# Performance work log

Hardware: AMD Instinct MI355X
Metric: run time of the kernel (lower is better)

Reference implementation:

```python
import jax, jax.numpy as jnp
import numpy as np


def _splat(img_bhwc, y0, y1, x0, x1):
    """Integral-image corner scatter: each source pixel adds its value over the
    inclusive rect [y0,y1]x[x0,x1] by writing signed deltas at 4 corners.
    The later double-cumsum turns these deltas into the box sums.
    Returns (count, img_acc) of shapes (b,h,w) and (b,h,w,c)."""
    b, h, w, c = img_bhwc.shape
    dt = img_bhwc.dtype
    y0c = jnp.maximum(y0, 0)
    x0c = jnp.maximum(x0, 0)
    yp = y1 + 1  # exclusive bottom row
    xp = x1 + 1  # exclusive right col
    my = (yp < h)
    mx = (xp < w)
    one = jnp.ones(y0c.shape, dt)
    zero = jnp.zeros(y0c.shape, dt)
    ypc = jnp.minimum(yp, h - 1)
    xpc = jnp.minimum(xp, w - 1)
    corners = [
        (y0c, x0c, one),
        (y0c, xpc, jnp.where(mx, -one, zero)),
        (ypc, x0c, jnp.where(my, -one, zero)),
        (ypc, xpc, jnp.where(my & mx, one, zero)),
    ]
    bidx = jnp.arange(b)[:, None, None]
    pix = img_bhwc.reshape(b * h * w, c)  # per-source-pixel splat value
    cnt = jnp.zeros((b * h * w,), dt)
    acc = jnp.zeros((b * h * w, c), dt)
    for yy, xx, wgt in corners:  # fixed 4-corner loop, not a data-dim loop
        idx = ((bidx * h + yy) * w + xx).reshape(-1)
        wf = wgt.reshape(-1)
        cnt = cnt.at[idx].add(wf)
        acc = acc.at[idx].add(wf[:, None] * pix)
    return cnt.reshape(b, h, w), acc.reshape(b, h, w, c)


def _finalize(cnt, img_acc):
    # integral image over (h, w), clamp count to >=1, average, clip to [0,1]
    cf = jnp.cumsum(jnp.cumsum(cnt, axis=1), axis=2)
    cf = jnp.maximum(cf, 1.0)
    av = jnp.cumsum(jnp.cumsum(img_acc, axis=1), axis=2) / cf[..., None]
    return jnp.clip(av, 0.0, 1.0)


def reference(image, depth):
    b, c, h, w = image.shape
    img = jnp.transpose(image, (0, 2, 3, 1))  # b,h,w,c
    R = jnp.floor(depth).astype(jnp.int32)  # splat radius in pixels (b,h,w)
    ys = jnp.arange(h)[:, None]
    xs = jnp.arange(w)[None, :]
    y0 = ys - R
    y1 = ys + R
    xc = jnp.broadcast_to(xs, R.shape)
    # left view: rect shifted left of the pixel; right view: shifted right
    cnt_l, acc_l = _splat(img, y0, y1, xc - 2 * R, xc)
    cnt_r, acc_r = _splat(img, y0, y1, xc, xc + 2 * R)
    img_left_avg = jnp.transpose(_finalize(cnt_l, acc_l), (0, 3, 1, 2))
    img_right_avg = jnp.transpose(_finalize(cnt_r, acc_r), (0, 3, 1, 2))
    return img_left_avg, img_right_avg


def setup_inputs() -> dict:
    key = jax.random.key(0)
    k1, k2 = jax.random.split(key)
    B, C, H, W = 8, 3, 1024, 1024
    MAX_DISP = 8.0  # max circle-of-confusion radius in pixels
    image = jax.random.uniform(k1, (B, C, H, W), dtype=jnp.float32)
    depth = jax.random.uniform(k2, (B, H, W), dtype=jnp.float32) * MAX_DISP
    return {"image": image, "depth": depth}
```

## Files before the change

### kernel.cpp

```cpp
#include <hip/hip_runtime.h>


typedef _Float16 h_t;
typedef _Float16 h4 __attribute__((ext_vector_type(4)));

constexpr int Hh = 1024, Ww = 1024, Bb = 8, Cc = 3;
constexpr int NCOL = 256;
constexpr int HALO = 14;
constexpr int TWD  = NCOL - 2 * HALO;
constexpr int STRIP = 32;
constexpr int RING = 17;

__device__ __forceinline__ float sat01(float x) {
  return fminf(fmaxf(x, 0.0f), 1.0f);
}

__device__ __forceinline__ int mod_ring(int y) {
  int m = y % RING;
  return m < 0 ? m + RING : m;
}

__global__ __launch_bounds__(256)
void coc_vsep(const float* __restrict__ img, const float* __restrict__ dep,
              float* __restrict__ out) {
  __shared__ h4 ring[RING * NCOL];
  __shared__ h4 Sb[8 * NCOL];

  const int c  = threadIdx.x;
  const int X0 = blockIdx.x * TWD;
  const int Y0 = blockIdx.y * STRIP;
  const int b  = blockIdx.z;
  const int x  = X0 - HALO + c;
  const size_t plane = (size_t)Hh * Ww;
  const float* db = dep + (size_t)b * plane;
  const float* ib = img + (size_t)b * Cc * plane;

  auto stage = [&](int y) {
    h4 v = {(h_t)0.f, (h_t)0.f, (h_t)0.f, (h_t)-1.f};
    if ((unsigned)y < (unsigned)Hh && (unsigned)x < (unsigned)Ww) {
      size_t p = (size_t)y * Ww + x;
      v.x = (h_t)ib[p];
      v.y = (h_t)ib[plane + p];
      v.z = (h_t)ib[2 * plane + p];
      v.w = (h_t)floorf(db[p]);
    }
    ring[mod_ring(y) * NCOL + c] = v;
  };

  for (int y = Y0 - 8; y <= Y0 + 8; ++y) stage(y);
  __syncthreads();

  float4 C[8];
  #pragma unroll
  for (int t = 0; t < 8; ++t) C[t] = make_float4(0.f, 0.f, 0.f, 0.f);
  #pragma unroll
  for (int d = -7; d <= 7; ++d) {
    h4 tx = ring[mod_ring(Y0 - 1 + d) * NCOL + c];
    float R = (float)tx.w;
    const int ad = d < 0 ? -d : d;
    #pragma unroll
    for (int t = ad; t < 8; ++t) {
      float m = sat01(1.0f - fabsf(R - (float)t));
      C[t].x = fmaf(m, (float)tx.x, C[t].x);
      C[t].y = fmaf(m, (float)tx.y, C[t].y);
      C[t].z = fmaf(m, (float)tx.z, C[t].z);
      C[t].w += m;
    }
  }

  int sY = mod_ring(Y0);
  for (int r = 0; r < STRIP; ++r) {
    const int Y = Y0 + r;

    #pragma unroll
    for (int t = 0; t < 8; ++t) {
      int si = sY + t;      si -= (si >= RING) ? RING : 0;
      int so = sY - 1 - t;  so += (so < 0) ? RING : 0;
      h4 ti = ring[si * NCOL + c];
      h4 to = ring[so * NCOL + c];
      float mi = sat01(1.0f - fabsf((float)ti.w - (float)t));
      float mo = sat01(1.0f - fabsf((float)to.w - (float)t));
      C[t].x = fmaf(mi, (float)ti.x, C[t].x);
      C[t].y = fmaf(mi, (float)ti.y, C[t].y);
      C[t].z = fmaf(mi, (float)ti.z, C[t].z);
      C[t].w += mi;
      C[t].x = fmaf(-mo, (float)to.x, C[t].x);
      C[t].y = fmaf(-mo, (float)to.y, C[t].y);
      C[t].z = fmaf(-mo, (float)to.z, C[t].z);
      C[t].w -= mo;
    }
    {
      float ax = 0.f, ay = 0.f, az = 0.f, aw = 0.f;
      #pragma unroll
      for (int t = 7; t >= 0; --t) {
        ax += C[t].x; ay += C[t].y; az += C[t].z; aw += C[t].w;
        h4 sv = {(h_t)ax, (h_t)ay, (h_t)az, (h_t)aw};
        Sb[t * NCOL + c] = sv;
      }
    }
    __syncthreads();

    if (c < TWD && (X0 + c) < Ww) {
      const int a = c + HALO;
      h4 s0 = Sb[0 * NCOL + a];
      float lx = (float)s0.x, ly = (float)s0.y, lz = (float)s0.z, lw = (float)s0.w;
      float rx = lx, ry = ly, rz = lz, rw = lw;
      #pragma unroll
      for (int k = 1; k <= 7; ++k) {
        h4 l0 = Sb[k * NCOL + a + 2 * k - 1];
        h4 l1 = Sb[k * NCOL + a + 2 * k];
        h4 r0 = Sb[k * NCOL + a - 2 * k];
        h4 r1 = Sb[k * NCOL + a - 2 * k + 1];
        lx += (float)l0.x + (float)l1.x;
        ly += (float)l0.y + (float)l1.y;
        lz += (float)l0.z + (float)l1.z;
        lw += (float)l0.w + (float)l1.w;
        rx += (float)r0.x + (float)r1.x;
        ry += (float)r0.y + (float)r1.y;
        rz += (float)r0.z + (float)r1.z;
        rw += (float)r0.w + (float)r1.w;
      }
      const int X = X0 + c;
      size_t p = (size_t)Y * Ww + X;
      float* outL = out + (size_t)b * Cc * plane;
      float* outR = out + (size_t)(Bb + b) * Cc * plane;
      float invL = 1.0f / fmaxf(lw, 1.0f);
      float invR = 1.0f / fmaxf(rw, 1.0f);
      outL[p]             = sat01(lx * invL);
      outL[plane + p]     = sat01(ly * invL);
      outL[2 * plane + p] = sat01(lz * invL);
      outR[p]             = sat01(rx * invR);
      outR[plane + p]     = sat01(ry * invR);
      outR[2 * plane + p] = sat01(rz * invR);
    }
    stage(Y + 9);
    __syncthreads();

    sY += 1; sY -= (sY >= RING) ? RING : 0;
  }
}

extern "C" void kernel_launch(void* const* d_in, const int* in_sizes, int n_in,
                              void* d_out, int out_size, void* d_ws, size_t ws_size,
                              hipStream_t stream) {
  const float* img = (const float*)d_in[0];
  const float* dep = (const float*)d_in[1];
  float* out = (float*)d_out;
  dim3 grid((Ww + TWD - 1) / TWD, Hh / STRIP, Bb);
  dim3 block(NCOL, 1, 1);
  hipLaunchKernelGGL(coc_vsep, grid, block, 0, stream, img, dep, out);
}
```

Before: 427.8 us.

## Replace shared-memory row ring with per-thread register sliding window

The 17-row shared-memory ring of staged pixels is replaced by a 16-entry per-thread register window, since each thread only reads its own column. The next row's global load is issued at the top of each iteration so it can overlap the accumulation. Depth is now held in fp32 registers instead of fp16. In exchange the kernel uses many more VGPRs for the window and register shifts, which may lower occupancy, and it keeps two barriers per row around the Sb writes.

Result: faster. 418.1 us (-2.3%).

```diff
diff --git a/kernel.cpp b/kernel.cpp
--- a/kernel.cpp
+++ b/kernel.cpp
@@ -9,21 +9,14 @@
 constexpr int HALO = 14;
 constexpr int TWD  = NCOL - 2 * HALO;
 constexpr int STRIP = 32;
-constexpr int RING = 17;
 
 __device__ __forceinline__ float sat01(float x) {
   return fminf(fmaxf(x, 0.0f), 1.0f);
 }
 
-__device__ __forceinline__ int mod_ring(int y) {
-  int m = y % RING;
-  return m < 0 ? m + RING : m;
-}
-
 __global__ __launch_bounds__(256)
 void coc_vsep(const float* __restrict__ img, const float* __restrict__ dep,
               float* __restrict__ out) {
-  __shared__ h4 ring[RING * NCOL];
   __shared__ h4 Sb[8 * NCOL];
 
   const int c  = threadIdx.x;
@@ -34,109 +27,119 @@
   const size_t plane = (size_t)Hh * Ww;
   const float* db = dep + (size_t)b * plane;
   const float* ib = img + (size_t)b * Cc * plane;
+  const bool xok = (unsigned)x < (unsigned)Ww;
 
-  auto stage = [&](int y) {
-    h4 v = {(h_t)0.f, (h_t)0.f, (h_t)0.f, (h_t)-1.f};
-    if ((unsigned)y < (unsigned)Hh && (unsigned)x < (unsigned)Ww) {
+  h4    Tc[16];
+  float Tr[16];
+
+  auto loadrow = [&](int y, h4& rgb, float& R) {
+    rgb = (h4){(h_t)0.f, (h_t)0.f, (h_t)0.f, (h_t)0.f};
+    R = -1.0f;
+    if ((unsigned)y < (unsigned)Hh && xok) {
       size_t p = (size_t)y * Ww + x;
-      v.x = (h_t)ib[p];
-      v.y = (h_t)ib[plane + p];
-      v.z = (h_t)ib[2 * plane + p];
-      v.w = (h_t)floorf(db[p]);
+      rgb.x = (h_t)ib[p];
+      rgb.y = (h_t)ib[plane + p];
+      rgb.z = (h_t)ib[2 * plane + p];
+      R = floorf(db[p]);
     }
-    ring[mod_ring(y) * NCOL + c] = v;
   };
 
-  for (int y = Y0 - 8; y <= Y0 + 8; ++y) stage(y);
-  __syncthreads();
+  #pragma unroll
+  for (int d = 0; d < 16; ++d) loadrow(Y0 - 8 + d, Tc[d], Tr[d]);
 
   float4 C[8];
   #pragma unroll
   for (int t = 0; t < 8; ++t) C[t] = make_float4(0.f, 0.f, 0.f, 0.f);
   #pragma unroll
   for (int d = -7; d <= 7; ++d) {
-    h4 tx = ring[mod_ring(Y0 - 1 + d) * NCOL + c];
-    float R = (float)tx.w;
+    const int i = 7 + d;
     const int ad = d < 0 ? -d : d;
     #pragma unroll
     for (int t = ad; t < 8; ++t) {
-      float m = sat01(1.0f - fabsf(R - (float)t));
-      C[t].x = fmaf(m, (float)tx.x, C[t].x);
-      C[t].y = fmaf(m, (float)tx.y, C[t].y);
-      C[t].z = fmaf(m, (float)tx.z, C[t].z);
+      float m = sat01(1.0f - fabsf(Tr[i] - (float)t));
+      C[t].x = fmaf(m, (float)Tc[i].x, C[t].x);
+      C[t].y = fmaf(m, (float)Tc[i].y, C[t].y);
+      C[t].z = fmaf(m, (float)Tc[i].z, C[t].z);
       C[t].w += m;
     }
   }
 
-  int sY = mod_ring(Y0);
+  float* outL = out + (size_t)b * Cc * plane;
+  float* outR = out + (size_t)(Bb + b) * Cc * plane;
+
+  #pragma unroll 2
   for (int r = 0; r < STRIP; ++r) {
     const int Y = Y0 + r;
+    h4 nc; float nr;
+    loadrow(Y + 8, nc, nr);
 
     #pragma unroll
     for (int t = 0; t < 8; ++t) {
-      int si = sY + t;      si -= (si >= RING) ? RING : 0;
-      int so = sY - 1 - t;  so += (so < 0) ? RING : 0;
-      h4 ti = ring[si * NCOL + c];
-      h4 to = ring[so * NCOL + c];
-      float mi = sat01(1.0f - fabsf((float)ti.w - (float)t));
-      float mo = sat01(1.0f - fabsf((float)to.w - (float)t));
-      C[t].x = fmaf(mi, (float)ti.x, C[t].x);
-      C[t].y = fmaf(mi, (float)ti.y, C[t].y);
-      C[t].z = fmaf(mi, (float)ti.z, C[t].z);
+      const int ii = 8 + t, io = 7 - t;
+      float mi = sat01(1.0f - fabsf(Tr[ii] - (float)t));
+      float mo = sat01(1.0f - fabsf(Tr[io] - (float)t));
+      C[t].x = fmaf(mi, (float)Tc[ii].x, C[t].x);
+      C[t].y = fmaf(mi, (float)Tc[ii].y, C[t].y);
+      C[t].z = fmaf(mi, (float)Tc[ii].z, C[t].z);
       C[t].w += mi;
-      C[t].x = fmaf(-mo, (float)to.x, C[t].x);
-      C[t].y = fmaf(-mo, (float)to.y, C[t].y);
-      C[t].z = fmaf(-mo, (float)to.z, C[t].z);
+      C[t].x = fmaf(-mo, (float)Tc[io].x, C[t].x);
+      C[t].y = fmaf(-mo, (float)Tc[io].y, C[t].y);
+      C[t].z = fmaf(-mo, (float)Tc[io].z, C[t].z);
       C[t].w -= mo;
     }
+
+    h4 sv[8];
     {
       float ax = 0.f, ay = 0.f, az = 0.f, aw = 0.f;
       #pragma unroll
       for (int t = 7; t >= 0; --t) {
         ax += C[t].x; ay += C[t].y; az += C[t].z; aw += C[t].w;
-        h4 sv = {(h_t)ax, (h_t)ay, (h_t)az, (h_t)aw};
-        Sb[t * NCOL + c] = sv;
+        sv[t] = (h4){(h_t)ax, (h_t)ay, (h_t)az, (h_t)aw};
       }
     }
+
+    __syncthreads();
+    #pragma unroll
+    for (int t = 0; t < 8; ++t) Sb[t * NCOL + c] = sv[t];
     __syncthreads();
 
     if (c < TWD && (X0 + c) < Ww) {
       const int a = c + HALO;
-      h4 s0 = Sb[0 * NCOL + a];
-      float lx = (float)s0.x, ly = (float)s0.y, lz = (float)s0.z, lw = (float)s0.w;
-      float rx = lx, ry = ly, rz = lz, rw = lw;
+      float4 L, Rv;
+      {
+        h4 s0 = Sb[a];
+        L.x = (float)s0.x; L.y = (float)s0.y; L.z = (float)s0.z; L.w = (float)s0.w;
+        Rv = L;
+      }
       #pragma unroll
       for (int k = 1; k <= 7; ++k) {
         h4 l0 = Sb[k * NCOL + a + 2 * k - 1];
         h4 l1 = Sb[k * NCOL + a + 2 * k];
         h4 r0 = Sb[k * NCOL + a - 2 * k];
         h4 r1 = Sb[k * NCOL + a - 2 * k + 1];
-        lx += (float)l0.x + (float)l1.x;
-        ly += (float)l0.y + (float)l1.y;
-        lz += (float)l0.z + (float)l1.z;
-        lw += (float)l0.w + (float)l1.w;
-        rx += (float)r0.x + (float)r1.x;
-        ry += (float)r0.y + (float)r1.y;
-        rz += (float)r0.z + (float)r1.z;
-        rw += (float)r0.w + (float)r1.w;
+        L.x += (float)l0.x + (float)l1.x;
+        L.y += (float)l0.y + (float)l1.y;
+        L.z += (float)l0.z + (float)l1.z;
+        L.w += (float)l0.w + (float)l1.w;
+        Rv.x += (float)r0.x + (float)r1.x;
+        Rv.y += (float)r0.y + (float)r1.y;
+        Rv.z += (float)r0.z + (float)r1.z;
+        Rv.w += (float)r0.w + (float)r1.w;
       }
-      const int X = X0 + c;
-      size_t p = (size_t)Y * Ww + X;
-      float* outL = out + (size_t)b * Cc * plane;
-      float* outR = out + (size_t)(Bb + b) * Cc * plane;
-      float invL = 1.0f / fmaxf(lw, 1.0f);
-      float invR = 1.0f / fmaxf(rw, 1.0f);
-      outL[p]             = sat01(lx * invL);
-      outL[plane + p]     = sat01(ly * invL);
-      outL[2 * plane + p] = sat01(lz * invL);
-      outR[p]             = sat01(rx * invR);
-      outR[plane + p]     = sat01(ry * invR);
-      outR[2 * plane + p] = sat01(rz * invR);
+      size_t p = (size_t)Y * Ww + (X0 + c);
+      float invL = 1.0f / fmaxf(L.w, 1.0f);
+      float invR = 1.0f / fmaxf(Rv.w, 1.0f);
+      outL[p]             = sat01(L.x * invL);
+      outL[plane + p]     = sat01(L.y * invL);
+      outL[2 * plane + p] = sat01(L.z * invL);
+      outR[p]             = sat01(Rv.x * invR);
+      outR[plane + p]     = sat01(Rv.y * invR);
+      outR[2 * plane + p] = sat01(Rv.z * invR);
     }
-    stage(Y + 9);
-    __syncthreads();
 
-    sY += 1; sY -= (sY >= RING) ? RING : 0;
+    #pragma unroll
+    for (int d = 0; d < 15; ++d) { Tc[d] = Tc[d + 1]; Tr[d] = Tr[d + 1]; }
+    Tc[15] = nc; Tr[15] = nr;
   }
 }
 
```
